# Kernel optimization log

Measured on AMD Instinct MI355X. Metric: run time of the kernel, lower is better.

## Reference

```python
import jax, jax.numpy as jnp
import numpy as np

N_NODES = 100000
N_EDGES = 1600000
N_GRAPHS = 1024
B = 1024
GNN_INP, GNN_HID, GNN_OUT = 64, 128, 64
INP, HID, OUT = 64, 256, 1
EPS = 1e-5  # torch BatchNorm1d default eps


def _bn(h, gamma, beta):
    # training-mode BatchNorm1d: biased batch statistics over dim 0
    m = h.mean(axis=0)
    v = jnp.mean((h - m) ** 2, axis=0)
    return (h - m) * jax.lax.rsqrt(v + EPS) * gamma + beta


def setup_inputs() -> dict:
    key = jax.random.key(0)
    ks = jax.random.split(key, 24)
    s = 0.05
    inp = {
        "x": jax.random.normal(ks[0], (B, INP), jnp.float32),
        "masks": jax.random.randint(ks[1], (B,), 0, N_GRAPHS),
        "gnn_x": jax.random.normal(ks[2], (N_NODES, GNN_INP), jnp.float32),
        "edge_index": jax.random.randint(ks[3], (2, N_EDGES), 0, N_NODES),
        "gnn_batch": jnp.sort(jax.random.randint(ks[4], (N_NODES,), 0, N_GRAPHS)),
        # GCNConv params
        "W_gcn": jax.random.normal(ks[5], (GNN_INP, GNN_HID), jnp.float32) * s,
        "b_gcn": jnp.zeros((GNN_HID,), jnp.float32),
        "g1": jnp.ones((GNN_HID,), jnp.float32), "be1": jnp.zeros((GNN_HID,), jnp.float32),
        "W_lin1": jax.random.normal(ks[6], (GNN_HID, GNN_HID // 2), jnp.float32) * s,
        "b_lin1": jnp.zeros((GNN_HID // 2,), jnp.float32),
        "g2": jnp.ones((GNN_HID // 2,), jnp.float32), "be2": jnp.zeros((GNN_HID // 2,), jnp.float32),
        "W_lin2": jax.random.normal(ks[7], (GNN_HID // 2, GNN_OUT), jnp.float32) * s,
        "b_lin2": jnp.zeros((GNN_OUT,), jnp.float32),
        "g3": jnp.ones((GNN_OUT,), jnp.float32), "be3": jnp.zeros((GNN_OUT,), jnp.float32),
        # head params
        "W_fc1": jax.random.normal(ks[8], (INP + GNN_OUT, HID), jnp.float32) * s,
        "b_fc1": jnp.zeros((HID,), jnp.float32),
        "g4": jnp.ones((HID,), jnp.float32), "be4": jnp.zeros((HID,), jnp.float32),
        "W_fc2": jax.random.normal(ks[9], (HID, HID // 4), jnp.float32) * s,
        "b_fc2": jnp.zeros((HID // 4,), jnp.float32),
        "g5": jnp.ones((HID // 4,), jnp.float32), "be5": jnp.zeros((HID // 4,), jnp.float32),
        "W_fc3": jax.random.normal(ks[10], (HID // 4, OUT), jnp.float32) * s,
        "b_fc3": jnp.zeros((OUT,), jnp.float32),
    }
    return inp


def _forward(x, masks, gnn_x, edge_index, gnn_batch,
             W_gcn, b_gcn, g1, be1, W_lin1, b_lin1, g2, be2, W_lin2, b_lin2,
             g3, be3, W_fc1, b_fc1, g4, be4, W_fc2, b_fc2, g5, be5, W_fc3, b_fc3):
    N = gnn_x.shape[0]
    # --- GCNConv: linear transform, self-loops, sym-normalized scatter-add ---
    h = gnn_x @ W_gcn  # [N, GNN_HID]
    loop = jnp.arange(N)
    src = jnp.concatenate([edge_index[0], loop])
    dst = jnp.concatenate([edge_index[1], loop])
    deg = jax.ops.segment_sum(jnp.ones_like(dst, jnp.float32), dst, num_segments=N)
    dis = jax.lax.rsqrt(deg)  # deg >= 1 thanks to self-loops
    norm = dis[src] * dis[dst]  # [E+N]
    agg = jax.ops.segment_sum(h[src] * norm[:, None], dst, num_segments=N) + b_gcn
    z = jax.nn.relu(_bn(agg, g1, be1))  # dropout = identity (eval)
    # --- global_mean_pool over graph ids ---
    sums = jax.ops.segment_sum(z, gnn_batch, num_segments=N_GRAPHS)
    cnt = jax.ops.segment_sum(jnp.ones((N,), jnp.float32), gnn_batch, num_segments=N_GRAPHS)
    pooled = sums / jnp.maximum(cnt, 1.0)[:, None]  # [G, GNN_HID]
    z = jax.nn.relu(_bn(pooled @ W_lin1 + b_lin1, g2, be2))
    z = _bn(z @ W_lin2 + b_lin2, g3, be3)  # [G, GNN_OUT]
    # --- MixGNN head ---
    g = z[masks]  # [B, GNN_OUT]
    t = jnp.concatenate([x, g], axis=1)
    t = jax.nn.relu(_bn(t @ W_fc1 + b_fc1, g4, be4))
    t = t * t  # Multiply([h, h])
    t = jax.nn.relu(_bn(t @ W_fc2 + b_fc2, g5, be5))
    t = t * t
    t = t * t
    return t @ W_fc3 + b_fc3  # [B, OUT]


def reference(x, masks, gnn_x, edge_index, gnn_batch,
              W_gcn, b_gcn, g1, be1, W_lin1, b_lin1, g2, be2, W_lin2, b_lin2,
              g3, be3, W_fc1, b_fc1, g4, be4, W_fc2, b_fc2, g5, be5, W_fc3, b_fc3):
    return _forward(x, masks, gnn_x, edge_index, gnn_batch,
                    W_gcn, b_gcn, g1, be1, W_lin1, b_lin1, g2, be2, W_lin2, b_lin2,
                    g3, be3, W_fc1, b_fc1, g4, be4, W_fc2, b_fc2, g5, be5, W_fc3, b_fc3)
```

## Files before the change

kernel.cpp:

```cpp
#include <hip/hip_runtime.h>
#include <hip/hip_bf16.h>

#define N_NODES 100000
#define N_EDGES 1600000
#define N_GRAPHS 1024
#define BSZ 1024
#define EPS 1e-5f

#define NBUCK 256
#define BUCKW 391
#define BCAP  8192
#define SRC_MASK 0x1FFFF
#define BIN_CHUNK 8192
#define BIN_BLOCKS 196
#define NCHUNK 512
#define CHUNK_ROWS 196

#define WS_STATS1  0
#define WS_STATS2  128
#define WS_STATS4  256
#define WS_STATS5  768
#define WS_ZTOTAL  896
#define WS_GCUR    896
#define WS_SCALE1  1152
#define WS_SHIFTP  1280
#define WS_M       1408
#define WS_COLSUM  5504
#define WS_GSTART  5568
#define WS_DIS     6596
#define WS_ROWPTR  106596
#define WS_ROWLEN  206596
#define WS_PACKED  306596
#define WS_MPART   306596
#define WS_CSRC    2403748
#define WS_CPART   2403748
#define WS_XH      4500900
#define WS_AGGX    7700900
#define WS_POOLED  14100900
#define WS_T1      14231972
#define WS_T2      14297508
#define WS_T4      14363044
#define WS_T5      14625188

__device__ inline unsigned short f2bf(float f) {
    unsigned int u = __float_as_uint(f);
    return (unsigned short)((u + 0x7FFFu + ((u >> 16) & 1u)) >> 16);
}

__global__ __launch_bounds__(256) void prep_kernel(float* __restrict__ ws,
                                                   const int* __restrict__ gbatch) {
    int b = blockIdx.x, tid = threadIdx.x;
    if (b == 0) {
        for (int i = tid; i < WS_ZTOTAL; i += 256) ws[i] = 0.0f;
    } else if (b == 1) {
        ((int*)(ws + WS_GCUR))[tid] = tid * BCAP;
    } else {
        int g = (b - 2) * 256 + tid;
        int lo = 0, hi = N_NODES;
        while (lo < hi) {
            int mid = (lo + hi) >> 1;
            if (gbatch[mid] < g) lo = mid + 1; else hi = mid;
        }
        int* gstart = (int*)(ws + WS_GSTART);
        gstart[g] = lo;
        if (g == 0) gstart[N_GRAPHS] = N_NODES;
    }
}

__global__ __launch_bounds__(256) void cvt_kernel(const float* __restrict__ x,
                                                  unsigned short* __restrict__ xh) {
    int i = blockIdx.x * 256 + threadIdx.x;
    float4 f = ((const float4*)x)[i];
    ushort4 h;
    h.x = f2bf(f.x); h.y = f2bf(f.y); h.z = f2bf(f.z); h.w = f2bf(f.w);
    ((ushort4*)xh)[i] = h;
}

__global__ __launch_bounds__(1024) void bin_kernel(const int* __restrict__ ei,
                                                   int* __restrict__ gcursor,
                                                   unsigned int* __restrict__ packed) {
    __shared__ unsigned int stage[BIN_CHUNK];
    __shared__ int lh[NBUCK], lbase[NBUCK], lcur[NBUCK], gb[NBUCK];
    const int* src = ei;
    const int* dst = ei + N_EDGES;
    int tid = threadIdx.x;
    int base = blockIdx.x * BIN_CHUNK;
    int n = min(BIN_CHUNK, N_EDGES - base);
    if (tid < NBUCK) lh[tid] = 0;
    __syncthreads();
    for (int i = tid; i < n; i += 1024)
        atomicAdd(&lh[dst[base + i] / BUCKW], 1);
    __syncthreads();
    if (tid < NBUCK) lbase[tid] = lh[tid];
    __syncthreads();
    for (int off = 1; off < NBUCK; off <<= 1) {
        int t = (tid < NBUCK && tid >= off) ? lbase[tid - off] : 0;
        __syncthreads();
        if (tid < NBUCK) lbase[tid] += t;
        __syncthreads();
    }
    if (tid < NBUCK) {
        int excl = lbase[tid] - lh[tid];
        lbase[tid] = excl;
        lcur[tid] = excl;
        gb[tid] = atomicAdd(&gcursor[tid], lh[tid]);
    }
    __syncthreads();
    for (int i = tid; i < n; i += 1024) {
        int d = dst[base + i];
        int s = src[base + i];
        int bk = d / BUCKW;
        int dl = d - bk * BUCKW;
        int slot = atomicAdd(&lcur[bk], 1);
        stage[slot] = ((unsigned int)dl << 17) | (unsigned int)s;
    }
    __syncthreads();
    int wid = tid >> 6, lane = tid & 63;
    for (int bk = wid; bk < NBUCK; bk += 16) {
        int lo = lbase[bk], go = gb[bk];
        int len = min(lh[bk], (bk + 1) * BCAP - go);
        for (int j = lane; j < len; j += 64)
            packed[go + j] = stage[lo + j];
    }
}

__global__ __launch_bounds__(256) void csr_build_kernel(const unsigned int* __restrict__ packed,
                                                        const int* __restrict__ gcur,
                                                        int* __restrict__ rowptr,
                                                        int* __restrict__ rowlen,
                                                        int* __restrict__ csrc,
                                                        float* __restrict__ dis) {
    __shared__ int dcnt[BUCKW];
    __shared__ int lcur[BUCKW];
    __shared__ int stage[BCAP];
    int b = blockIdx.x, tid = threadIdx.x;
    int e0 = b * BCAP;
    int ecnt = min(gcur[b] - e0, BCAP);
    int nbase = b * BUCKW;
    int nmax = min(BUCKW, N_NODES - nbase);
    for (int i = tid; i < BUCKW; i += 256) dcnt[i] = 0;
    __syncthreads();
    for (int i = tid; i < ecnt; i += 256)
        atomicAdd(&dcnt[packed[e0 + i] >> 17], 1);
    __syncthreads();
    for (int i = tid; i < nmax; i += 256) {
        dis[nbase + i] = rsqrtf((float)dcnt[i] + 1.0f);
        rowlen[nbase + i] = dcnt[i];
    }
    __syncthreads();
    if (tid < 64) {
        int lane = tid;
        int run = 0;
        for (int c = 0; c < BUCKW; c += 64) {
            int idx = c + lane;
            int v = (idx < BUCKW) ? dcnt[idx] : 0;
            int inc = v;
#pragma unroll
            for (int off = 1; off < 64; off <<= 1) {
                int t = __shfl_up(inc, off);
                if (lane >= off) inc += t;
            }
            if (idx < BUCKW) {
                int excl = run + inc - v;
                dcnt[idx] = excl;
                lcur[idx] = excl;
            }
            run += __shfl(inc, 63);
        }
    }
    __syncthreads();
    for (int i = tid; i < nmax; i += 256)
        rowptr[nbase + i] = e0 + dcnt[i];
    for (int i = tid; i < ecnt; i += 256) {
        unsigned int r = packed[e0 + i];
        int slot = atomicAdd(&lcur[r >> 17], 1);
        stage[slot] = (int)(r & SRC_MASK);
    }
    __syncthreads();
    for (int i = tid; i < ecnt; i += 256) csrc[e0 + i] = stage[i];
}

__global__ __launch_bounds__(256) void gather_kernel(const unsigned short* __restrict__ xh,
                                                     const int* __restrict__ rowptr,
                                                     const int* __restrict__ rowlen,
                                                     const int* __restrict__ csrc,
                                                     const float* __restrict__ dis,
                                                     float* __restrict__ aggx) {
    int wid = (blockIdx.x * 256 + threadIdx.x) >> 6;
    int lane = threadIdx.x & 63;
    if (wid >= N_NODES) return;
    int start = rowptr[wid];
    int len = rowlen[wid];
    float dd = dis[wid];
    float self = __uint_as_float((unsigned int)xh[(size_t)wid * 64 + lane] << 16);
    float acc = self * dd * dd;
    for (int j0 = 0; j0 < len; j0 += 64) {
        int cnt = min(64, len - j0);
        int sv = 0;
        float wv = 0.f;
        if (lane < cnt) {
            sv = csrc[start + j0 + lane];
            wv = dis[sv] * dd;
        }
        int iters = (cnt + 7) & ~7;
        for (int k = 0; k < iters; k += 8) {
            int s[8]; float w[8], v[8];
#pragma unroll
            for (int u = 0; u < 8; ++u) {
                s[u] = __shfl(sv, k + u);
                w[u] = __shfl(wv, k + u);
            }
#pragma unroll
            for (int u = 0; u < 8; ++u)
                v[u] = __uint_as_float((unsigned int)xh[(size_t)s[u] * 64 + lane] << 16);
#pragma unroll
            for (int u = 0; u < 8; ++u) acc = fmaf(v[u], w[u], acc);
        }
    }
    aggx[(size_t)wid * 64 + lane] = acc;
}

__global__ __launch_bounds__(256) void moment_kernel(const float* __restrict__ aggx,
                                                     float* __restrict__ mpart,
                                                     float* __restrict__ cpart) {
    __shared__ float rows[8 * 64];
    int c = blockIdx.x, tid = threadIdx.x;
    int r0 = c * CHUNK_ROWS;
    int r1 = min(r0 + CHUNK_ROWS, N_NODES);
    int i0 = (tid >> 6) * 16;
    int j = tid & 63;
    float acc[16] = {};
    float cs = 0.f;
    for (int it = 0; it < (CHUNK_ROWS + 7) / 8; ++it) {
        int sid = tid * 2;
        int grow = r0 + it * 8 + (sid >> 6);
        float2 v = {0.f, 0.f};
        if (grow < r1) v = *(const float2*)(aggx + (size_t)(r0 + it * 8) * 64 + sid);
        __syncthreads();
        *(float2*)(rows + sid) = v;
        __syncthreads();
#pragma unroll
        for (int rr = 0; rr < 8; ++rr) {
            float bj = rows[rr * 64 + j];
            float4 a0 = *(const float4*)(rows + rr * 64 + i0);
            float4 a1 = *(const float4*)(rows + rr * 64 + i0 + 4);
            float4 a2 = *(const float4*)(rows + rr * 64 + i0 + 8);
            float4 a3 = *(const float4*)(rows + rr * 64 + i0 + 12);
            acc[0]  += a0.x * bj; acc[1]  += a0.y * bj; acc[2]  += a0.z * bj; acc[3]  += a0.w * bj;
            acc[4]  += a1.x * bj; acc[5]  += a1.y * bj; acc[6]  += a1.z * bj; acc[7]  += a1.w * bj;
            acc[8]  += a2.x * bj; acc[9]  += a2.y * bj; acc[10] += a2.z * bj; acc[11] += a2.w * bj;
            acc[12] += a3.x * bj; acc[13] += a3.y * bj; acc[14] += a3.z * bj; acc[15] += a3.w * bj;
        }
        if (tid < 64) {
#pragma unroll
            for (int rr = 0; rr < 8; ++rr) cs += rows[rr * 64 + tid];
        }
    }
#pragma unroll
    for (int m = 0; m < 16; ++m)
        mpart[(size_t)c * 4096 + (i0 + m) * 64 + j] = acc[m];
    if (tid < 64) cpart[c * 64 + tid] = cs;
}

__global__ __launch_bounds__(128) void mreduce_kernel(const float* __restrict__ mpart,
                                                      float* __restrict__ M) {
    int idx = blockIdx.x * 128 + threadIdx.x;
    float s = 0.f;
#pragma unroll 8
    for (int c = 0; c < NCHUNK; ++c) s += mpart[(size_t)c * 4096 + idx];
    M[idx] = s;
}

__global__ __launch_bounds__(256) void fold_kernel(const float* __restrict__ M,
                                                   const float* __restrict__ cpart,
                                                   const float* __restrict__ W,
                                                   const float* __restrict__ g1,
                                                   const float* __restrict__ be1,
                                                   float* __restrict__ scale1,
                                                   float* __restrict__ shiftp) {
    __shared__ float Ml[4096];
    __shared__ float sl[64];
    __shared__ float sp[4][64];
    __shared__ float qh[2][128];
    int tid = threadIdx.x;
#pragma unroll
    for (int m = 0; m < 16; ++m) Ml[m * 256 + tid] = M[m * 256 + tid];
    {
        int i = tid & 63, q4 = tid >> 6;
        float s = 0.f;
        for (int c = q4 * (NCHUNK / 4); c < (q4 + 1) * (NCHUNK / 4); ++c)
            s += cpart[c * 64 + i];
        sp[q4][i] = s;
    }
    __syncthreads();
    if (tid < 64) sl[tid] = sp[0][tid] + sp[1][tid] + sp[2][tid] + sp[3][tid];
    __syncthreads();
    int j = tid & 127, half = tid >> 7;
    float wv[64];
#pragma unroll
    for (int k = 0; k < 64; ++k) wv[k] = W[k * 128 + j];
    float q = 0.f;
    for (int i = half * 32; i < half * 32 + 32; ++i) {
        float ti = 0.f;
#pragma unroll
        for (int k = 0; k < 64; ++k) ti += Ml[i * 64 + k] * wv[k];
        q += ti * wv[i];
    }
    qh[half][j] = q;
    __syncthreads();
    if (tid < 128) {
        float Ey2 = (qh[0][j] + qh[1][j]) * (1.0f / N_NODES);
        float my = 0.f;
#pragma unroll
        for (int k = 0; k < 64; ++k) my += sl[k] * wv[k];
        my *= (1.0f / N_NODES);
        float var = Ey2 - my * my;
        float sc = g1[j] * rsqrtf(var + EPS);
        scale1[j] = sc;
        shiftp[j] = be1[j] - my * sc;
    }
}

__global__ __launch_bounds__(256) void pool_kernel(const float* __restrict__ aggx,
                                                   const int* __restrict__ gstart,
                                                   const float* __restrict__ W,
                                                   const float* __restrict__ scale1,
                                                   const float* __restrict__ shiftp,
                                                   float* __restrict__ pooled) {
    __shared__ float rows[128];
    __shared__ float pp[256];
    int gph = blockIdx.x, tid = threadIdx.x;
    int c = tid & 127, rg = tid >> 7;
    float wreg[64];
#pragma unroll
    for (int k = 0; k < 64; ++k) wreg[k] = W[k * 128 + c];
    float sc = scale1[c], sh = shiftp[c];
    int r0 = gstart[gph], r1 = gstart[gph + 1];
    float acc = 0.f;
    for (int rb = r0; rb < r1; rb += 2) {
        __syncthreads();
        if (tid < 128) {
            int rr = rb + (tid >> 6);
            rows[tid] = (rr < r1) ? aggx[(size_t)rr * 64 + (tid & 63)] : 0.f;
        }
        __syncthreads();
        int r = rb + rg;
        if (r < r1) {
            float y = 0.f;
            const float4* rv = (const float4*)(rows + rg * 64);
#pragma unroll
            for (int k4 = 0; k4 < 16; ++k4) {
                float4 v = rv[k4];
                y += v.x * wreg[k4 * 4] + v.y * wreg[k4 * 4 + 1]
                   + v.z * wreg[k4 * 4 + 2] + v.w * wreg[k4 * 4 + 3];
            }
            acc += fmaxf(y * sc + sh, 0.f);
        }
    }
    pp[tid] = acc;
    __syncthreads();
    if (tid < 128) {
        int cnt = r1 - r0;
        float inv = 1.0f / fmaxf((float)cnt, 1.0f);
        pooled[(size_t)gph * 128 + c] = (pp[c] + pp[128 + c]) * inv;
    }
}

__global__ __launch_bounds__(256) void lin1_kernel(const float* __restrict__ pooled,
                                                   const float* __restrict__ W,
                                                   const float* __restrict__ bias,
                                                   float* __restrict__ t1,
                                                   float* __restrict__ stats1) {
    __shared__ float ls[256], ls2[256];
    int tid = threadIdx.x;
    int r = blockIdx.x * 4 + (tid >> 6);
    int c = tid & 63;
    float acc = bias[c];
    const float* srow = pooled + (size_t)r * 128;
#pragma unroll 8
    for (int k = 0; k < 128; ++k)
        acc += srow[k] * W[k * 64 + c];
    t1[r * 64 + c] = acc;
    ls[tid] = acc; ls2[tid] = acc * acc;
    __syncthreads();
    if (tid < 64) {
        float s = ls[tid] + ls[tid + 64] + ls[tid + 128] + ls[tid + 192];
        float q = ls2[tid] + ls2[tid + 64] + ls2[tid + 128] + ls2[tid + 192];
        unsafeAtomicAdd(&stats1[c], s);
        unsafeAtomicAdd(&stats1[64 + c], q);
    }
}

__global__ __launch_bounds__(256) void lin2_kernel(const float* __restrict__ t1,
                                                   const float* __restrict__ stats1,
                                                   const float* __restrict__ g,
                                                   const float* __restrict__ be,
                                                   const float* __restrict__ W,
                                                   const float* __restrict__ bias,
                                                   float* __restrict__ t2,
                                                   float* __restrict__ stats2) {
    __shared__ float sc[64], sh[64];
    __shared__ float ls[256], ls2[256];
    int tid = threadIdx.x;
    if (tid < 64) {
        float m = stats1[tid] * (1.0f / BSZ);
        float var = stats1[64 + tid] * (1.0f / BSZ) - m * m;
        float s = g[tid] * rsqrtf(var + EPS);
        sc[tid] = s; sh[tid] = be[tid] - m * s;
    }
    __syncthreads();
    int r = blockIdx.x * 4 + (tid >> 6);
    int c = tid & 63;
    float acc = bias[c];
    const float* row = t1 + (size_t)r * 64;
#pragma unroll 8
    for (int k = 0; k < 64; ++k) {
        float z = fmaxf(row[k] * sc[k] + sh[k], 0.f);
        acc += z * W[k * 64 + c];
    }
    t2[r * 64 + c] = acc;
    ls[tid] = acc; ls2[tid] = acc * acc;
    __syncthreads();
    if (tid < 64) {
        float s = ls[tid] + ls[tid + 64] + ls[tid + 128] + ls[tid + 192];
        float q = ls2[tid] + ls2[tid + 64] + ls2[tid + 128] + ls2[tid + 192];
        unsafeAtomicAdd(&stats2[c], s);
        unsafeAtomicAdd(&stats2[64 + c], q);
    }
}

__global__ __launch_bounds__(1024) void fc1_kernel(const float* __restrict__ x,
                                                   const int* __restrict__ masks,
                                                   const float* __restrict__ t2,
                                                   const float* __restrict__ stats2,
                                                   const float* __restrict__ g3,
                                                   const float* __restrict__ be3,
                                                   const float* __restrict__ W,
                                                   const float* __restrict__ bias,
                                                   float* __restrict__ t4,
                                                   float* __restrict__ stats4) {
    __shared__ float sc[64], sh[64];
    __shared__ float cat[4][128];
    __shared__ float ls[1024], ls2[1024];
    int tid = threadIdx.x;
    if (tid < 64) {
        float m = stats2[tid] * (1.0f / BSZ);
        float var = stats2[64 + tid] * (1.0f / BSZ) - m * m;
        float s = g3[tid] * rsqrtf(var + EPS);
        sc[tid] = s; sh[tid] = be3[tid] - m * s;
    }
    __syncthreads();
    int r0 = blockIdx.x * 4;
    if (tid < 512) {
        int i = tid >> 7;
        int k = tid & 127;
        int r = r0 + i;
        float v;
        if (k < 64) {
            v = x[r * 64 + k];
        } else {
            int mrow = masks[r];
            int kk = k - 64;
            v = t2[mrow * 64 + kk] * sc[kk] + sh[kk];
        }
        cat[i][k] = v;
    }
    __syncthreads();
    int i = tid >> 8;
    int c = tid & 255;
    float acc = bias[c];
#pragma unroll 8
    for (int k = 0; k < 128; ++k)
        acc += cat[i][k] * W[k * 256 + c];
    t4[(size_t)(r0 + i) * 256 + c] = acc;
    ls[tid] = acc; ls2[tid] = acc * acc;
    __syncthreads();
    if (tid < 256) {
        float s = ls[tid] + ls[tid + 256] + ls[tid + 512] + ls[tid + 768];
        float q = ls2[tid] + ls2[tid + 256] + ls2[tid + 512] + ls2[tid + 768];
        unsafeAtomicAdd(&stats4[c], s);
        unsafeAtomicAdd(&stats4[256 + c], q);
    }
}

__global__ __launch_bounds__(256) void fc2_kernel(const float* __restrict__ t4,
                                                  const float* __restrict__ stats4,
                                                  const float* __restrict__ g4,
                                                  const float* __restrict__ be4,
                                                  const float* __restrict__ W,
                                                  const float* __restrict__ bias,
                                                  float* __restrict__ t5,
                                                  float* __restrict__ stats5) {
    __shared__ float sc[256], sh[256];
    __shared__ float ls[256], ls2[256];
    int tid = threadIdx.x;
    {
        float m = stats4[tid] * (1.0f / BSZ);
        float var = stats4[256 + tid] * (1.0f / BSZ) - m * m;
        float s = g4[tid] * rsqrtf(var + EPS);
        sc[tid] = s; sh[tid] = be4[tid] - m * s;
    }
    __syncthreads();
    int r = blockIdx.x * 4 + (tid >> 6);
    int c = tid & 63;
    float acc = bias[c];
    const float* row = t4 + (size_t)r * 256;
#pragma unroll 8
    for (int k = 0; k < 256; ++k) {
        float z = fmaxf(row[k] * sc[k] + sh[k], 0.f);
        z *= z;
        acc += z * W[k * 64 + c];
    }
    t5[r * 64 + c] = acc;
    ls[tid] = acc; ls2[tid] = acc * acc;
    __syncthreads();
    if (tid < 64) {
        float s = ls[tid] + ls[tid + 64] + ls[tid + 128] + ls[tid + 192];
        float q = ls2[tid] + ls2[tid + 64] + ls2[tid + 128] + ls2[tid + 192];
        unsafeAtomicAdd(&stats5[c], s);
        unsafeAtomicAdd(&stats5[64 + c], q);
    }
}

__global__ __launch_bounds__(256) void fc3_kernel(const float* __restrict__ t5,
                                                  const float* __restrict__ stats5,
                                                  const float* __restrict__ g5,
                                                  const float* __restrict__ be5,
                                                  const float* __restrict__ W,
                                                  const float* __restrict__ bias,
                                                  float* __restrict__ out) {
    __shared__ float sc[64], sh[64];
    int tid = threadIdx.x;
    if (tid < 64) {
        float m = stats5[tid] * (1.0f / BSZ);
        float var = stats5[64 + tid] * (1.0f / BSZ) - m * m;
        float s = g5[tid] * rsqrtf(var + EPS);
        sc[tid] = s; sh[tid] = be5[tid] - m * s;
    }
    __syncthreads();
    int r = blockIdx.x * 256 + tid;
    float acc = bias[0];
    const float* row = t5 + (size_t)r * 64;
#pragma unroll
    for (int k = 0; k < 64; ++k) {
        float z = fmaxf(row[k] * sc[k] + sh[k], 0.f);
        z = z * z;
        z = z * z;
        acc += z * W[k];
    }
    out[r] = acc;
}

extern "C" void kernel_launch(void* const* d_in, const int* in_sizes, int n_in,
                              void* d_out, int out_size, void* d_ws, size_t ws_size,
                              hipStream_t stream) {
    const float* x      = (const float*)d_in[0];
    const int*   masks  = (const int*)d_in[1];
    const float* gnn_x  = (const float*)d_in[2];
    const int*   ei     = (const int*)d_in[3];
    const int*   gbatch = (const int*)d_in[4];
    const float* W_gcn  = (const float*)d_in[5];
    const float* b_gcn  = (const float*)d_in[6];
    const float* g1     = (const float*)d_in[7];
    const float* be1    = (const float*)d_in[8];
    const float* W_lin1 = (const float*)d_in[9];
    const float* b_lin1 = (const float*)d_in[10];
    const float* g2     = (const float*)d_in[11];
    const float* be2    = (const float*)d_in[12];
    const float* W_lin2 = (const float*)d_in[13];
    const float* b_lin2 = (const float*)d_in[14];
    const float* g3     = (const float*)d_in[15];
    const float* be3    = (const float*)d_in[16];
    const float* W_fc1  = (const float*)d_in[17];
    const float* b_fc1  = (const float*)d_in[18];
    const float* g4     = (const float*)d_in[19];
    const float* be4    = (const float*)d_in[20];
    const float* W_fc2  = (const float*)d_in[21];
    const float* b_fc2  = (const float*)d_in[22];
    const float* g5     = (const float*)d_in[23];
    const float* be5    = (const float*)d_in[24];
    const float* W_fc3  = (const float*)d_in[25];
    const float* b_fc3  = (const float*)d_in[26];
    (void)b_gcn;

    float* ws = (float*)d_ws;
    float* stats1 = ws + WS_STATS1;
    float* stats2 = ws + WS_STATS2;
    float* stats4 = ws + WS_STATS4;
    float* stats5 = ws + WS_STATS5;
    int*   gcur   = (int*)(ws + WS_GCUR);
    float* scale1 = ws + WS_SCALE1;
    float* shiftp = ws + WS_SHIFTP;
    float* Mbuf   = ws + WS_M;
    int*   gstart = (int*)(ws + WS_GSTART);
    float* dis    = ws + WS_DIS;
    int*   rowptr = (int*)(ws + WS_ROWPTR);
    int*   rowlen = (int*)(ws + WS_ROWLEN);
    unsigned int* packed = (unsigned int*)(ws + WS_PACKED);
    float* mpart  = ws + WS_MPART;
    int*   csrc   = (int*)(ws + WS_CSRC);
    float* cpart  = ws + WS_CPART;
    unsigned short* xh = (unsigned short*)(ws + WS_XH);
    float* aggx   = ws + WS_AGGX;
    float* pooled = ws + WS_POOLED;
    float* t1     = ws + WS_T1;
    float* t2     = ws + WS_T2;
    float* t4     = ws + WS_T4;
    float* t5     = ws + WS_T5;
    float* out    = (float*)d_out;

    prep_kernel<<<6, 256, 0, stream>>>(ws, gbatch);
    cvt_kernel<<<N_NODES * 64 / 4 / 256, 256, 0, stream>>>(gnn_x, xh);
    bin_kernel<<<BIN_BLOCKS, 1024, 0, stream>>>(ei, gcur, packed);
    csr_build_kernel<<<NBUCK, 256, 0, stream>>>(packed, gcur, rowptr, rowlen, csrc, dis);
    gather_kernel<<<(N_NODES * 64 + 255) / 256, 256, 0, stream>>>(xh, rowptr, rowlen, csrc, dis, aggx);
    moment_kernel<<<NCHUNK, 256, 0, stream>>>(aggx, mpart, cpart);
    mreduce_kernel<<<32, 128, 0, stream>>>(mpart, Mbuf);
    fold_kernel<<<1, 256, 0, stream>>>(Mbuf, cpart, W_gcn, g1, be1, scale1, shiftp);
    pool_kernel<<<N_GRAPHS, 256, 0, stream>>>(aggx, gstart, W_gcn, scale1, shiftp, pooled);
    lin1_kernel<<<256, 256, 0, stream>>>(pooled, W_lin1, b_lin1, t1, stats1);
    lin2_kernel<<<256, 256, 0, stream>>>(t1, stats1, g2, be2, W_lin2, b_lin2, t2, stats2);
    fc1_kernel<<<256, 1024, 0, stream>>>(x, masks, t2, stats2, g3, be3, W_fc1, b_fc1, t4, stats4);
    fc2_kernel<<<256, 256, 0, stream>>>(t4, stats4, g4, be4, W_fc2, b_fc2, t5, stats5);
    fc3_kernel<<<4, 256, 0, stream>>>(t5, stats5, g5, be5, W_fc3, b_fc3, out);
}
```

Before: 280.3 us.

## Replace per-graph pooling with row-tiled GEMM+atomic pool; atomically reduce moments

The per-graph pool kernel (one block per graph, serial over rows) is replaced by a row-tiled kernel that computes relu(BN(aggx@W)) for 16 nodes per block and accumulates segment sums with atomics into a zeroed psum buffer. The mean division is moved into lin1. Moment partials are now atomically accumulated directly, which removes the mreduce kernel and the cpart reduction in fold. The bin and CSR kernels are also rebalanced to smaller chunks and more blocks, and prep zeroes the larger workspace across 16 blocks. This is meant to fix load imbalance and add parallelism, at the cost of atomic contention and non-deterministic float sums.

```diff
diff --git a/kernel.cpp b/kernel.cpp
--- a/kernel.cpp
+++ b/kernel.cpp
@@ -11,32 +11,30 @@
 #define BUCKW 391
 #define BCAP  8192
 #define SRC_MASK 0x1FFFF
-#define BIN_CHUNK 8192
-#define BIN_BLOCKS 196
+#define BIN_CHUNK 4096
+#define BIN_BLOCKS 391
 #define NCHUNK 512
 #define CHUNK_ROWS 196
 
-#define WS_STATS1  0
-#define WS_STATS2  128
-#define WS_STATS4  256
-#define WS_STATS5  768
-#define WS_ZTOTAL  896
-#define WS_GCUR    896
-#define WS_SCALE1  1152
-#define WS_SHIFTP  1280
-#define WS_M       1408
-#define WS_COLSUM  5504
-#define WS_GSTART  5568
-#define WS_DIS     6596
-#define WS_ROWPTR  106596
-#define WS_ROWLEN  206596
-#define WS_PACKED  306596
-#define WS_MPART   306596
-#define WS_CSRC    2403748
-#define WS_CPART   2403748
-#define WS_XH      4500900
-#define WS_AGGX    7700900
-#define WS_POOLED  14100900
+#define WS_PSUM    0
+#define WS_STATS1  131072
+#define WS_STATS2  131200
+#define WS_STATS4  131328
+#define WS_STATS5  131840
+#define WS_M       131968
+#define WS_CS      136064
+#define WS_ZTOTAL  136128
+#define WS_GCUR    136128
+#define WS_SCALE1  136384
+#define WS_SHIFTP  136512
+#define WS_GSTART  136640
+#define WS_DIS     137668
+#define WS_ROWPTR  237668
+#define WS_ROWLEN  337668
+#define WS_PACKED  437668
+#define WS_CSRC    2534820
+#define WS_XH      4631972
+#define WS_AGGX    7831972
 #define WS_T1      14231972
 #define WS_T2      14297508
 #define WS_T4      14363044
@@ -50,12 +48,12 @@
 __global__ __launch_bounds__(256) void prep_kernel(float* __restrict__ ws,
                                                    const int* __restrict__ gbatch) {
     int b = blockIdx.x, tid = threadIdx.x;
-    if (b == 0) {
-        for (int i = tid; i < WS_ZTOTAL; i += 256) ws[i] = 0.0f;
-    } else if (b == 1) {
+    if (b < 16) {
+        for (int i = b * 256 + tid; i < WS_ZTOTAL; i += 16 * 256) ws[i] = 0.0f;
+    } else if (b == 16) {
         ((int*)(ws + WS_GCUR))[tid] = tid * BCAP;
     } else {
-        int g = (b - 2) * 256 + tid;
+        int g = (b - 17) * 256 + tid;
         int lo = 0, hi = N_NODES;
         while (lo < hi) {
             int mid = (lo + hi) >> 1;
@@ -76,9 +74,9 @@
     ((ushort4*)xh)[i] = h;
 }
 
-__global__ __launch_bounds__(1024) void bin_kernel(const int* __restrict__ ei,
-                                                   int* __restrict__ gcursor,
-                                                   unsigned int* __restrict__ packed) {
+__global__ __launch_bounds__(512) void bin_kernel(const int* __restrict__ ei,
+                                                  int* __restrict__ gcursor,
+                                                  unsigned int* __restrict__ packed) {
     __shared__ unsigned int stage[BIN_CHUNK];
     __shared__ int lh[NBUCK], lbase[NBUCK], lcur[NBUCK], gb[NBUCK];
     const int* src = ei;
@@ -88,7 +86,7 @@
     int n = min(BIN_CHUNK, N_EDGES - base);
     if (tid < NBUCK) lh[tid] = 0;
     __syncthreads();
-    for (int i = tid; i < n; i += 1024)
+    for (int i = tid; i < n; i += 512)
         atomicAdd(&lh[dst[base + i] / BUCKW], 1);
     __syncthreads();
     if (tid < NBUCK) lbase[tid] = lh[tid];
@@ -106,7 +104,7 @@
         gb[tid] = atomicAdd(&gcursor[tid], lh[tid]);
     }
     __syncthreads();
-    for (int i = tid; i < n; i += 1024) {
+    for (int i = tid; i < n; i += 512) {
         int d = dst[base + i];
         int s = src[base + i];
         int bk = d / BUCKW;
@@ -116,7 +114,7 @@
     }
     __syncthreads();
     int wid = tid >> 6, lane = tid & 63;
-    for (int bk = wid; bk < NBUCK; bk += 16) {
+    for (int bk = wid; bk < NBUCK; bk += 8) {
         int lo = lbase[bk], go = gb[bk];
         int len = min(lh[bk], (bk + 1) * BCAP - go);
         for (int j = lane; j < len; j += 64)
@@ -124,7 +122,7 @@
     }
 }
 
-__global__ __launch_bounds__(256) void csr_build_kernel(const unsigned int* __restrict__ packed,
+__global__ __launch_bounds__(512) void csr_build_kernel(const unsigned int* __restrict__ packed,
                                                         const int* __restrict__ gcur,
                                                         int* __restrict__ rowptr,
                                                         int* __restrict__ rowlen,
@@ -138,12 +136,12 @@
     int ecnt = min(gcur[b] - e0, BCAP);
     int nbase = b * BUCKW;
     int nmax = min(BUCKW, N_NODES - nbase);
-    for (int i = tid; i < BUCKW; i += 256) dcnt[i] = 0;
-    __syncthreads();
-    for (int i = tid; i < ecnt; i += 256)
+    for (int i = tid; i < BUCKW; i += 512) dcnt[i] = 0;
+    __syncthreads();
+    for (int i = tid; i < ecnt; i += 512)
         atomicAdd(&dcnt[packed[e0 + i] >> 17], 1);
     __syncthreads();
-    for (int i = tid; i < nmax; i += 256) {
+    for (int i = tid; i < nmax; i += 512) {
         dis[nbase + i] = rsqrtf((float)dcnt[i] + 1.0f);
         rowlen[nbase + i] = dcnt[i];
     }
@@ -169,15 +167,15 @@
         }
     }
     __syncthreads();
-    for (int i = tid; i < nmax; i += 256)
+    for (int i = tid; i < nmax; i += 512)
         rowptr[nbase + i] = e0 + dcnt[i];
-    for (int i = tid; i < ecnt; i += 256) {
+    for (int i = tid; i < ecnt; i += 512) {
         unsigned int r = packed[e0 + i];
         int slot = atomicAdd(&lcur[r >> 17], 1);
         stage[slot] = (int)(r & SRC_MASK);
     }
     __syncthreads();
-    for (int i = tid; i < ecnt; i += 256) csrc[e0 + i] = stage[i];
+    for (int i = tid; i < ecnt; i += 512) csrc[e0 + i] = stage[i];
 }
 
 __global__ __launch_bounds__(256) void gather_kernel(const unsigned short* __restrict__ xh,
@@ -221,8 +219,8 @@
 }
 
 __global__ __launch_bounds__(256) void moment_kernel(const float* __restrict__ aggx,
-                                                     float* __restrict__ mpart,
-                                                     float* __restrict__ cpart) {
+                                                     float* __restrict__ M,
+                                                     float* __restrict__ CS) {
     __shared__ float rows[8 * 64];
     int c = blockIdx.x, tid = threadIdx.x;
     int r0 = c * CHUNK_ROWS;
@@ -258,21 +256,12 @@
     }
 #pragma unroll
     for (int m = 0; m < 16; ++m)
-        mpart[(size_t)c * 4096 + (i0 + m) * 64 + j] = acc[m];
-    if (tid < 64) cpart[c * 64 + tid] = cs;
-}
-
-__global__ __launch_bounds__(128) void mreduce_kernel(const float* __restrict__ mpart,
-                                                      float* __restrict__ M) {
-    int idx = blockIdx.x * 128 + threadIdx.x;
-    float s = 0.f;
-#pragma unroll 8
-    for (int c = 0; c < NCHUNK; ++c) s += mpart[(size_t)c * 4096 + idx];
-    M[idx] = s;
+        unsafeAtomicAdd(&M[(i0 + m) * 64 + j], acc[m]);
+    if (tid < 64) unsafeAtomicAdd(&CS[tid], cs);
 }
 
 __global__ __launch_bounds__(256) void fold_kernel(const float* __restrict__ M,
-                                                   const float* __restrict__ cpart,
+                                                   const float* __restrict__ CS,
                                                    const float* __restrict__ W,
                                                    const float* __restrict__ g1,
                                                    const float* __restrict__ be1,
@@ -280,20 +269,11 @@
                                                    float* __restrict__ shiftp) {
     __shared__ float Ml[4096];
     __shared__ float sl[64];
-    __shared__ float sp[4][64];
     __shared__ float qh[2][128];
     int tid = threadIdx.x;
 #pragma unroll
     for (int m = 0; m < 16; ++m) Ml[m * 256 + tid] = M[m * 256 + tid];
-    {
-        int i = tid & 63, q4 = tid >> 6;
-        float s = 0.f;
-        for (int c = q4 * (NCHUNK / 4); c < (q4 + 1) * (NCHUNK / 4); ++c)
-            s += cpart[c * 64 + i];
-        sp[q4][i] = s;
-    }
-    __syncthreads();
-    if (tid < 64) sl[tid] = sp[0][tid] + sp[1][tid] + sp[2][tid] + sp[3][tid];
+    if (tid < 64) sl[tid] = CS[tid];
     __syncthreads();
     int j = tid & 127, half = tid >> 7;
     float wv[64];
@@ -321,52 +301,69 @@
     }
 }
 
-__global__ __launch_bounds__(256) void pool_kernel(const float* __restrict__ aggx,
+__global__ __launch_bounds__(256) void gemm_pool_kernel(const float* __restrict__ aggx,
+                                                        const int* __restrict__ gbatch,
+                                                        const float* __restrict__ W,
+                                                        const float* __restrict__ scale1,
+                                                        const float* __restrict__ shiftp,
+                                                        float* __restrict__ psum) {
+    __shared__ float Ws[64 * 128];
+    __shared__ float As[16 * 64];
+    __shared__ float Zs[16 * 128];
+    __shared__ int gid[16];
+    int tid = threadIdx.x;
+    const float4* W4 = (const float4*)W;
+    float4* Ws4 = (float4*)Ws;
+#pragma unroll
+    for (int i = 0; i < 8; ++i) Ws4[tid + i * 256] = W4[tid + i * 256];
+    int row0 = blockIdx.x * 16;
+    ((float4*)As)[tid] = ((const float4*)(aggx + (size_t)row0 * 64))[tid];
+    if (tid < 16) gid[tid] = gbatch[row0 + tid];
+    __syncthreads();
+    int tx = tid & 31;
+    int ty = tid >> 5;
+    int r0 = ty * 2;
+    float4 sc4 = ((const float4*)scale1)[tx];
+    float4 sh4 = ((const float4*)shiftp)[tx];
+    float acc[2][4] = {};
+#pragma unroll
+    for (int k = 0; k < 64; ++k) {
+        float a0 = As[r0 * 64 + k];
+        float a1 = As[(r0 + 1) * 64 + k];
+        float4 w = Ws4[k * 32 + tx];
+        acc[0][0] += a0 * w.x; acc[0][1] += a0 * w.y; acc[0][2] += a0 * w.z; acc[0][3] += a0 * w.w;
+        acc[1][0] += a1 * w.x; acc[1][1] += a1 * w.y; acc[1][2] += a1 * w.z; acc[1][3] += a1 * w.w;
+    }
+#pragma unroll
+    for (int rr = 0; rr < 2; ++rr) {
+        float4 z;
+        z.x = fmaxf(acc[rr][0] * sc4.x + sh4.x, 0.f);
+        z.y = fmaxf(acc[rr][1] * sc4.y + sh4.y, 0.f);
+        z.z = fmaxf(acc[rr][2] * sc4.z + sh4.z, 0.f);
+        z.w = fmaxf(acc[rr][3] * sc4.w + sh4.w, 0.f);
+        ((float4*)(Zs + (r0 + rr) * 128))[tx] = z;
+    }
+    __syncthreads();
+    if (tid < 128) {
+        int c = tid;
+        float a = 0.f;
+        int g = gid[0];
+#pragma unroll
+        for (int i = 0; i < 16; ++i) {
+            int gi = gid[i];
+            if (gi != g) {
+                unsafeAtomicAdd(&psum[(size_t)g * 128 + c], a);
+                a = 0.f;
+                g = gi;
+            }
+            a += Zs[i * 128 + c];
+        }
+        unsafeAtomicAdd(&psum[(size_t)g * 128 + c], a);
+    }
+}
+
+__global__ __launch_bounds__(256) void lin1_kernel(const float* __restrict__ psum,
                                                    const int* __restrict__ gstart,
-                                                   const float* __restrict__ W,
-                                                   const float* __restrict__ scale1,
-                                                   const float* __restrict__ shiftp,
-                                                   float* __restrict__ pooled) {
-    __shared__ float rows[128];
-    __shared__ float pp[256];
-    int gph = blockIdx.x, tid = threadIdx.x;
-    int c = tid & 127, rg = tid >> 7;
-    float wreg[64];
-#pragma unroll
-    for (int k = 0; k < 64; ++k) wreg[k] = W[k * 128 + c];
-    float sc = scale1[c], sh = shiftp[c];
-    int r0 = gstart[gph], r1 = gstart[gph + 1];
-    float acc = 0.f;
-    for (int rb = r0; rb < r1; rb += 2) {
-        __syncthreads();
-        if (tid < 128) {
-            int rr = rb + (tid >> 6);
-            rows[tid] = (rr < r1) ? aggx[(size_t)rr * 64 + (tid & 63)] : 0.f;
-        }
-        __syncthreads();
-        int r = rb + rg;
-        if (r < r1) {
-            float y = 0.f;
-            const float4* rv = (const float4*)(rows + rg * 64);
-#pragma unroll
-            for (int k4 = 0; k4 < 16; ++k4) {
-                float4 v = rv[k4];
-                y += v.x * wreg[k4 * 4] + v.y * wreg[k4 * 4 + 1]
-                   + v.z * wreg[k4 * 4 + 2] + v.w * wreg[k4 * 4 + 3];
-            }
-            acc += fmaxf(y * sc + sh, 0.f);
-        }
-    }
-    pp[tid] = acc;
-    __syncthreads();
-    if (tid < 128) {
-        int cnt = r1 - r0;
-        float inv = 1.0f / fmaxf((float)cnt, 1.0f);
-        pooled[(size_t)gph * 128 + c] = (pp[c] + pp[128 + c]) * inv;
-    }
-}
-
-__global__ __launch_bounds__(256) void lin1_kernel(const float* __restrict__ pooled,
                                                    const float* __restrict__ W,
                                                    const float* __restrict__ bias,
                                                    float* __restrict__ t1,
@@ -375,11 +372,13 @@
     int tid = threadIdx.x;
     int r = blockIdx.x * 4 + (tid >> 6);
     int c = tid & 63;
-    float acc = bias[c];
-    const float* srow = pooled + (size_t)r * 128;
+    float invc = 1.0f / fmaxf((float)(gstart[r + 1] - gstart[r]), 1.0f);
+    float acc = 0.f;
+    const float* srow = psum + (size_t)r * 128;
 #pragma unroll 8
     for (int k = 0; k < 128; ++k)
         acc += srow[k] * W[k * 64 + c];
+    acc = bias[c] + acc * invc;
     t1[r * 64 + c] = acc;
     ls[tid] = acc; ls2[tid] = acc * acc;
     __syncthreads();
@@ -584,41 +583,39 @@
     (void)b_gcn;
 
     float* ws = (float*)d_ws;
+    float* psum   = ws + WS_PSUM;
     float* stats1 = ws + WS_STATS1;
     float* stats2 = ws + WS_STATS2;
     float* stats4 = ws + WS_STATS4;
     float* stats5 = ws + WS_STATS5;
+    float* Mbuf   = ws + WS_M;
+    float* CSbuf  = ws + WS_CS;
     int*   gcur   = (int*)(ws + WS_GCUR);
     float* scale1 = ws + WS_SCALE1;
     float* shiftp = ws + WS_SHIFTP;
-    float* Mbuf   = ws + WS_M;
     int*   gstart = (int*)(ws + WS_GSTART);
     float* dis    = ws + WS_DIS;
     int*   rowptr = (int*)(ws + WS_ROWPTR);
     int*   rowlen = (int*)(ws + WS_ROWLEN);
     unsigned int* packed = (unsigned int*)(ws + WS_PACKED);
-    float* mpart  = ws + WS_MPART;
     int*   csrc   = (int*)(ws + WS_CSRC);
-    float* cpart  = ws + WS_CPART;
     unsigned short* xh = (unsigned short*)(ws + WS_XH);
     float* aggx   = ws + WS_AGGX;
-    float* pooled = ws + WS_POOLED;
     float* t1     = ws + WS_T1;
     float* t2     = ws + WS_T2;
     float* t4     = ws + WS_T4;
     float* t5     = ws + WS_T5;
     float* out    = (float*)d_out;
 
-    prep_kernel<<<6, 256, 0, stream>>>(ws, gbatch);
+    prep_kernel<<<21, 256, 0, stream>>>(ws, gbatch);
     cvt_kernel<<<N_NODES * 64 / 4 / 256, 256, 0, stream>>>(gnn_x, xh);
-    bin_kernel<<<BIN_BLOCKS, 1024, 0, stream>>>(ei, gcur, packed);
-    csr_build_kernel<<<NBUCK, 256, 0, stream>>>(packed, gcur, rowptr, rowlen, csrc, dis);
+    bin_kernel<<<BIN_BLOCKS, 512, 0, stream>>>(ei, gcur, packed);
+    csr_build_kernel<<<NBUCK, 512, 0, stream>>>(packed, gcur, rowptr, rowlen, csrc, dis);
     gather_kernel<<<(N_NODES * 64 + 255) / 256, 256, 0, stream>>>(xh, rowptr, rowlen, csrc, dis, aggx);
-    moment_kernel<<<NCHUNK, 256, 0, stream>>>(aggx, mpart, cpart);
-    mreduce_kernel<<<32, 128, 0, stream>>>(mpart, Mbuf);
-    fold_kernel<<<1, 256, 0, stream>>>(Mbuf, cpart, W_gcn, g1, be1, scale1, shiftp);
-    pool_kernel<<<N_GRAPHS, 256, 0, stream>>>(aggx, gstart, W_gcn, scale1, shiftp, pooled);
-    lin1_kernel<<<256, 256, 0, stream>>>(pooled, W_lin1, b_lin1, t1, stats1);
+    moment_kernel<<<NCHUNK, 256, 0, stream>>>(aggx, Mbuf, CSbuf);
+    fold_kernel<<<1, 256, 0, stream>>>(Mbuf, CSbuf, W_gcn, g1, be1, scale1, shiftp);
+    gemm_pool_kernel<<<N_NODES / 16, 256, 0, stream>>>(aggx, gbatch, W_gcn, scale1, shiftp, psum);
+    lin1_kernel<<<256, 256, 0, stream>>>(psum, gstart, W_lin1, b_lin1, t1, stats1);
     lin2_kernel<<<256, 256, 0, stream>>>(t1, stats1, g2, be2, W_lin2, b_lin2, t2, stats2);
     fc1_kernel<<<256, 1024, 0, stream>>>(x, masks, t2, stats2, g3, be3, W_fc1, b_fc1, t4, stats4);
     fc2_kernel<<<256, 256, 0, stream>>>(t4, stats4, g4, be4, W_fc2, b_fc2, t5, stats5);
```

After: 254.7 us. 9.1% less time.
